# Performance work log

Measured on AMD Instinct MI355X. Metric: run time of the kernel, lower is better.

Reference implementation:

```python
import jax, jax.numpy as jnp
import numpy as np

B, H, W, C = 64, 56, 56, 256
ROUTES = 4
CONV_OUT = 64
BN_EPS = 1e-3  # keras BatchNormalization default epsilon


def setup_inputs() -> dict:
    key = jax.random.key(0)
    ks = jax.random.split(key, 8)
    inputs = jax.random.normal(ks[0], (B, H, W, C), jnp.float32)
    gamma = jnp.ones((C,), jnp.float32)
    beta = jnp.zeros((C,), jnp.float32)
    moving_mean = 0.1 * jax.random.normal(ks[1], (C,), jnp.float32)
    moving_var = jax.random.uniform(ks[2], (C,), jnp.float32, 0.5, 1.5)
    conv_w = 0.02 * jax.random.normal(ks[3], (3, 3, C, CONV_OUT), jnp.float32)  # HWIO
    conv_b = jnp.zeros((CONV_OUT,), jnp.float32)
    fc_w = 0.05 * jax.random.normal(ks[4], (CONV_OUT, ROUTES), jnp.float32)
    fc_b = jnp.zeros((ROUTES,), jnp.float32)
    return {"inputs": inputs, "gamma": gamma, "beta": beta,
            "moving_mean": moving_mean, "moving_var": moving_var,
            "conv_w": conv_w, "conv_b": conv_b, "fc_w": fc_w, "fc_b": fc_b}


def reference(inputs, gamma, beta, moving_mean, moving_var, conv_w, conv_b, fc_w, fc_b):
    # BatchNormalization in inference mode (training=None -> moving stats)
    rx = (inputs - moving_mean) * jax.lax.rsqrt(moving_var + BN_EPS) * gamma + beta
    # Conv2D(64, 3x3, stride 2, padding 'same'), NHWC / HWIO
    rx = jax.lax.conv_general_dilated(
        rx, conv_w, window_strides=(2, 2), padding="SAME",
        dimension_numbers=("NHWC", "HWIO", "NHWC")) + conv_b
    # GlobalAveragePooling2D -> [B, 64]
    rx = jnp.mean(rx, axis=(1, 2))
    # Dense(routes) -> routing logits [B, ROUTES]
    routing_x = rx @ fc_w + fc_b
    # choose_route: top-1 route, direct per-sample channel slice (no dense mask)
    route_width = C // ROUTES
    route = jnp.argmax(routing_x, axis=-1)  # [B]
    ch_idx = route[:, None] * route_width + jnp.arange(route_width)  # [B, rw]
    idx = ch_idx[:, None, None, :]  # [B,1,1,rw] broadcasts over H, W
    x = jnp.take_along_axis(inputs, idx, axis=3)  # [B, H, W, rw]
    return x, routing_x
```

## Files before the change

### kernel.cpp

```cpp
#include <hip/hip_runtime.h>

#define B 64
#define H 56
#define W 56
#define C 256
#define ROUTES 4
#define CONV_OUT 64
#define BN_EPS 0.001f
#define RW (C / ROUTES)
#define X_SIZE ((long)B * H * W * RW)

#define WS_FLOATS ((long)B * H * 3 * C)

typedef float floatx4 __attribute__((ext_vector_type(4)));

__device__ __forceinline__ void f4add(float4& a, const float4& v) {
    a.x += v.x; a.y += v.y; a.z += v.z; a.w += v.w;
}

__global__ __launch_bounds__(256) void k_reduce(const float* __restrict__ x,
                                                float* __restrict__ ws) {
    int blk = blockIdx.x;
    int tid = threadIdx.x;
    int cg = tid & 63;
    int wg = tid >> 6;

    const float4* xv = (const float4*)x;
    long base = (long)blk * W * (C / 4) + cg;

    float4 v[14];
    #pragma unroll
    for (int i = 0; i < 14; ++i) v[i] = xv[base + (long)(wg + 4 * i) * (C / 4)];

    float4 a = {0,0,0,0}, b4 = {0,0,0,0};
    #pragma unroll
    for (int i = 0; i < 14; i += 2) { f4add(a, v[i]); f4add(b4, v[i + 1]); }
    f4add(a, b4);

    __shared__ float4 lds[4][64];
    lds[wg][cg] = a;

    float4* w3 = (float4*)ws + (long)blk * 3 * (C / 4);
    if (wg == 0) w3[2 * (C / 4) + cg] = v[0];
    __syncthreads();
    if (wg == 0) {
        float4 e = lds[0][cg]; f4add(e, lds[2][cg]);
        w3[cg] = e;
    } else if (wg == 1) {
        float4 o = lds[1][cg]; f4add(o, lds[3][cg]);
        w3[C / 4 + cg] = o;
    }
}

__global__ __launch_bounds__(256) void k_route(const float* __restrict__ ws,
                                               const float* __restrict__ gamma,
                                               const float* __restrict__ beta,
                                               const float* __restrict__ mmean,
                                               const float* __restrict__ mvar,
                                               const float* __restrict__ conv_w,
                                               const float* __restrict__ conv_b,
                                               const float* __restrict__ fc_w,
                                               const float* __restrict__ fc_b,
                                               float* __restrict__ out_routing,
                                               int* __restrict__ route) {
    __shared__ float tl[9][C];
    __shared__ float part[4][CONV_OUT];
    __shared__ float cm[CONV_OUT];
    __shared__ float rxs[ROUTES];

    int b = blockIdx.x;
    int c = threadIdx.x;

    const float* base = ws + (long)b * H * 3 * C;
    float See = 0, Seo = 0, Soe = 0, Soo = 0, c0e = 0, c0o = 0;
    for (int h = 0; h < H; h += 2) {
        const float* pe = base + (long)h * 3 * C;
        const float* po = pe + 3 * C;
        See += pe[c];          Seo += pe[C + c];     c0e += pe[2 * C + c];
        Soe += po[c];          Soo += po[C + c];     c0o += po[2 * C + c];
    }
    float r0e = base[c];
    float r0o = base[C + c];
    float x00 = base[2 * C + c];

    float a  = gamma[c] * rsqrtf(mvar[c] + BN_EPS);
    float bb = beta[c] - mmean[c] * a;

    float Sx[9] = { See,             Seo,             See - c0e,
                    Soe,             Soo,             Soe - c0o,
                    See - r0e,       Seo - r0o,       See - r0e - c0e + x00 };
    const float cnt[9] = { 784.f, 784.f, 756.f,
                           784.f, 784.f, 756.f,
                           756.f, 756.f, 729.f };
    #pragma unroll
    for (int k = 0; k < 9; ++k) tl[k][c] = a * Sx[k] + bb * cnt[k];
    __syncthreads();

    int o = threadIdx.x & 63;
    int g = threadIdx.x >> 6;
    float p = 0.f;
    for (int cc = g * 64; cc < g * 64 + 64; ++cc) {
        #pragma unroll
        for (int k = 0; k < 9; ++k)
            p += tl[k][cc] * conv_w[(k * C + cc) * CONV_OUT + o];
    }
    part[g][o] = p;
    __syncthreads();

    if (threadIdx.x < CONV_OUT) {
        int o2 = threadIdx.x;
        float s = part[0][o2] + part[1][o2] + part[2][o2] + part[3][o2];
        cm[o2] = s * (1.f / 784.f) + conv_b[o2];
    }
    __syncthreads();

    if (threadIdx.x < ROUTES) {
        int r = threadIdx.x;
        float s = fc_b[r];
        for (int o2 = 0; o2 < CONV_OUT; ++o2) s += cm[o2] * fc_w[o2 * ROUTES + r];
        rxs[r] = s;
        out_routing[b * ROUTES + r] = s;
    }
    __syncthreads();

    if (threadIdx.x == 0) {
        int best = 0;
        for (int r = 1; r < ROUTES; ++r) if (rxs[r] > rxs[best]) best = r;
        route[b] = best;
    }
}

__global__ __launch_bounds__(256) void k_gather(const float* __restrict__ x,
                                                const int* __restrict__ route,
                                                float* __restrict__ out) {
    long idx = (long)blockIdx.x * blockDim.x + threadIdx.x;
    int j = (int)(idx & 15);
    long pixel = idx >> 4;
    int b = (int)(pixel / (H * W));
    const floatx4* xv = (const floatx4*)x;
    floatx4 v = xv[pixel * (C / 4) + (long)route[b] * (RW / 4) + j];
    __builtin_nontemporal_store(v, &((floatx4*)out)[idx]);
}

extern "C" void kernel_launch(void* const* d_in, const int* in_sizes, int n_in,
                              void* d_out, int out_size, void* d_ws, size_t ws_size,
                              hipStream_t stream) {
    const float* inputs = (const float*)d_in[0];
    const float* gamma  = (const float*)d_in[1];
    const float* beta   = (const float*)d_in[2];
    const float* mmean  = (const float*)d_in[3];
    const float* mvar   = (const float*)d_in[4];
    const float* conv_w = (const float*)d_in[5];
    const float* conv_b = (const float*)d_in[6];
    const float* fc_w   = (const float*)d_in[7];
    const float* fc_b   = (const float*)d_in[8];

    float* out   = (float*)d_out;
    float* ws    = (float*)d_ws;
    int*   route = (int*)((char*)d_ws + WS_FLOATS * sizeof(float));

    k_reduce<<<B * H, 256, 0, stream>>>(inputs, ws);
    k_route<<<B, 256, 0, stream>>>(ws, gamma, beta, mmean, mvar,
                                   conv_w, conv_b, fc_w, fc_b,
                                   out + X_SIZE, route);
    long n4 = X_SIZE / 4;
    k_gather<<<(int)(n4 / 256), 256, 0, stream>>>(inputs, route, out);
}
```

Before: 354.0 us.

## Fold conv and dense weights into per-channel route coefficients, atomically accumulate partial sums

Precomputes a fused weight that folds the conv weights through the dense layer and the BN scale, so each channel maps directly to four route logits. These weights are computed in four extra blocks of the reduce kernel. Per-row partial sums are accumulated with atomics into a compact per-batch 9xC buffer instead of a per-row workspace, which shrinks the route kernel to a short dot product and tree reduction. The gather kernel now does four vectors per thread and loads the route once per block. The atomic traffic and the added memset launch are the costs, and float atomics make the summation order nondeterministic.

New measurement: 331.2 us. 1.07x faster.

```diff
diff --git a/kernel.cpp b/kernel.cpp
--- a/kernel.cpp
+++ b/kernel.cpp
@@ -10,7 +10,10 @@
 #define RW (C / ROUTES)
 #define X_SIZE ((long)B * H * W * RW)
 
-#define WS_FLOATS ((long)B * H * 3 * C)
+#define P_FLOATS ((long)B * 9 * C)
+#define OFFU P_FLOATS
+#define U_FLOATS (10L * C * 4)
+#define OFFROUTE (OFFU + U_FLOATS)
 
 typedef float floatx4 __attribute__((ext_vector_type(4)));
 
@@ -19,9 +22,67 @@
 }
 
 __global__ __launch_bounds__(256) void k_reduce(const float* __restrict__ x,
+                                                const float* __restrict__ gamma,
+                                                const float* __restrict__ beta,
+                                                const float* __restrict__ mmean,
+                                                const float* __restrict__ mvar,
+                                                const float* __restrict__ conv_w,
+                                                const float* __restrict__ fc_w,
                                                 float* __restrict__ ws) {
+    int tid = threadIdx.x;
+
+    if (blockIdx.x >= B * H) {
+        __shared__ float fcw_s[CONV_OUT * ROUTES];
+        fcw_s[tid] = fc_w[tid];
+        __syncthreads();
+
+        int c = (blockIdx.x - B * H) * 64 + (tid >> 2);
+        int r = tid & 3;
+
+        float t[9];
+        #pragma unroll
+        for (int k = 0; k < 9; ++k) {
+            const float4* w4 = (const float4*)conv_w + ((long)(k * C + c) * CONV_OUT) / 4;
+            float s = 0.f;
+            #pragma unroll
+            for (int o4 = 0; o4 < 16; ++o4) {
+                float4 wv = w4[o4];
+                s += wv.x * fcw_s[(o4 * 4 + 0) * 4 + r];
+                s += wv.y * fcw_s[(o4 * 4 + 1) * 4 + r];
+                s += wv.z * fcw_s[(o4 * 4 + 2) * 4 + r];
+                s += wv.w * fcw_s[(o4 * 4 + 3) * 4 + r];
+            }
+            t[k] = s;
+        }
+
+        float a  = gamma[c] * rsqrtf(mvar[c] + BN_EPS);
+        float bb = beta[c] - mmean[c] * a;
+
+        float u[10];
+        u[0] =  t[0] + t[2] + t[6] + t[8];
+        u[1] =  t[1] + t[7];
+        u[2] =  t[3] + t[5];
+        u[3] =  t[4];
+        u[4] = -(t[2] + t[8]);
+        u[5] = -t[5];
+        u[6] = -(t[6] + t[8]);
+        u[7] = -t[7];
+        u[8] =  t[8];
+        u[9] = 784.f * (t[0] + t[1] + t[3] + t[4])
+             + 756.f * (t[2] + t[5] + t[6] + t[7])
+             + 729.f * t[8];
+
+        float* U = ws + OFFU;
+        float sa = a * (1.f / 784.f);
+        #pragma unroll
+        for (int j = 0; j < 9; ++j) U[(j * C + c) * 4 + r] = sa * u[j];
+        U[(9 * C + c) * 4 + r] = bb * (1.f / 784.f) * u[9];
+        return;
+    }
+
     int blk = blockIdx.x;
-    int tid = threadIdx.x;
+    int b = blk / H;
+    int h = blk % H;
     int cg = tid & 63;
     int wg = tid >> 6;
 
@@ -32,98 +93,70 @@
     #pragma unroll
     for (int i = 0; i < 14; ++i) v[i] = xv[base + (long)(wg + 4 * i) * (C / 4)];
 
-    float4 a = {0,0,0,0}, b4 = {0,0,0,0};
-    #pragma unroll
-    for (int i = 0; i < 14; i += 2) { f4add(a, v[i]); f4add(b4, v[i + 1]); }
-    f4add(a, b4);
+    float4 a4 = {0,0,0,0}, b4 = {0,0,0,0};
+    #pragma unroll
+    for (int i = 0; i < 14; i += 2) { f4add(a4, v[i]); f4add(b4, v[i + 1]); }
+    f4add(a4, b4);
 
     __shared__ float4 lds[4][64];
-    lds[wg][cg] = a;
-
-    float4* w3 = (float4*)ws + (long)blk * 3 * (C / 4);
-    if (wg == 0) w3[2 * (C / 4) + cg] = v[0];
+    lds[wg][cg] = a4;
     __syncthreads();
+
+    float* Pb = ws + (long)b * 9 * C;
+    int c0 = cg * 4;
+    int hp = h & 1;
+    #define ATOM4(j, q) { float* p = Pb + (j) * C + c0; \
+        atomicAdd(p+0, (q).x); atomicAdd(p+1, (q).y); \
+        atomicAdd(p+2, (q).z); atomicAdd(p+3, (q).w); }
+
     if (wg == 0) {
         float4 e = lds[0][cg]; f4add(e, lds[2][cg]);
-        w3[cg] = e;
+        ATOM4(hp * 2, e);
+        ATOM4(4 + hp, v[0]);
+        if (h == 0) { ATOM4(6, e); ATOM4(8, v[0]); }
     } else if (wg == 1) {
         float4 o = lds[1][cg]; f4add(o, lds[3][cg]);
-        w3[C / 4 + cg] = o;
-    }
+        ATOM4(hp * 2 + 1, o);
+        if (h == 0) ATOM4(7, o);
+    }
+    #undef ATOM4
 }
 
 __global__ __launch_bounds__(256) void k_route(const float* __restrict__ ws,
-                                               const float* __restrict__ gamma,
-                                               const float* __restrict__ beta,
-                                               const float* __restrict__ mmean,
-                                               const float* __restrict__ mvar,
-                                               const float* __restrict__ conv_w,
                                                const float* __restrict__ conv_b,
                                                const float* __restrict__ fc_w,
                                                const float* __restrict__ fc_b,
                                                float* __restrict__ out_routing,
                                                int* __restrict__ route) {
-    __shared__ float tl[9][C];
-    __shared__ float part[4][CONV_OUT];
-    __shared__ float cm[CONV_OUT];
+    __shared__ floatx4 red[256];
     __shared__ float rxs[ROUTES];
 
     int b = blockIdx.x;
     int c = threadIdx.x;
-
-    const float* base = ws + (long)b * H * 3 * C;
-    float See = 0, Seo = 0, Soe = 0, Soo = 0, c0e = 0, c0o = 0;
-    for (int h = 0; h < H; h += 2) {
-        const float* pe = base + (long)h * 3 * C;
-        const float* po = pe + 3 * C;
-        See += pe[c];          Seo += pe[C + c];     c0e += pe[2 * C + c];
-        Soe += po[c];          Soo += po[C + c];     c0o += po[2 * C + c];
-    }
-    float r0e = base[c];
-    float r0o = base[C + c];
-    float x00 = base[2 * C + c];
-
-    float a  = gamma[c] * rsqrtf(mvar[c] + BN_EPS);
-    float bb = beta[c] - mmean[c] * a;
-
-    float Sx[9] = { See,             Seo,             See - c0e,
-                    Soe,             Soo,             Soe - c0o,
-                    See - r0e,       Seo - r0o,       See - r0e - c0e + x00 };
-    const float cnt[9] = { 784.f, 784.f, 756.f,
-                           784.f, 784.f, 756.f,
-                           756.f, 756.f, 729.f };
-    #pragma unroll
-    for (int k = 0; k < 9; ++k) tl[k][c] = a * Sx[k] + bb * cnt[k];
+    const float* Pb = ws + (long)b * 9 * C;
+    const floatx4* U4 = (const floatx4*)(ws + OFFU);
+
+    floatx4 v = U4[9 * C + c];
+    #pragma unroll
+    for (int j = 0; j < 9; ++j) v += Pb[j * C + c] * U4[j * C + c];
+
+    red[c] = v;
     __syncthreads();
-
-    int o = threadIdx.x & 63;
-    int g = threadIdx.x >> 6;
-    float p = 0.f;
-    for (int cc = g * 64; cc < g * 64 + 64; ++cc) {
-        #pragma unroll
-        for (int k = 0; k < 9; ++k)
-            p += tl[k][cc] * conv_w[(k * C + cc) * CONV_OUT + o];
-    }
-    part[g][o] = p;
+    #pragma unroll
+    for (int s = 128; s >= 1; s >>= 1) {
+        if (c < s) red[c] += red[c + s];
+        __syncthreads();
+    }
+
+    if (c < ROUTES) {
+        float cst = fc_b[c];
+        for (int o = 0; o < CONV_OUT; ++o) cst += conv_b[o] * fc_w[o * ROUTES + c];
+        float val = red[0][c] + cst;
+        rxs[c] = val;
+        out_routing[b * ROUTES + c] = val;
+    }
     __syncthreads();
-
-    if (threadIdx.x < CONV_OUT) {
-        int o2 = threadIdx.x;
-        float s = part[0][o2] + part[1][o2] + part[2][o2] + part[3][o2];
-        cm[o2] = s * (1.f / 784.f) + conv_b[o2];
-    }
-    __syncthreads();
-
-    if (threadIdx.x < ROUTES) {
-        int r = threadIdx.x;
-        float s = fc_b[r];
-        for (int o2 = 0; o2 < CONV_OUT; ++o2) s += cm[o2] * fc_w[o2 * ROUTES + r];
-        rxs[r] = s;
-        out_routing[b * ROUTES + r] = s;
-    }
-    __syncthreads();
-
-    if (threadIdx.x == 0) {
+    if (c == 0) {
         int best = 0;
         for (int r = 1; r < ROUTES; ++r) if (rxs[r] > rxs[best]) best = r;
         route[b] = best;
@@ -133,13 +166,18 @@
 __global__ __launch_bounds__(256) void k_gather(const float* __restrict__ x,
                                                 const int* __restrict__ route,
                                                 float* __restrict__ out) {
-    long idx = (long)blockIdx.x * blockDim.x + threadIdx.x;
-    int j = (int)(idx & 15);
-    long pixel = idx >> 4;
-    int b = (int)(pixel / (H * W));
+    long base4 = (long)blockIdx.x * 1024 + threadIdx.x;
+    int b = blockIdx.x / 49;
+    int rt = route[b];
     const floatx4* xv = (const floatx4*)x;
-    floatx4 v = xv[pixel * (C / 4) + (long)route[b] * (RW / 4) + j];
-    __builtin_nontemporal_store(v, &((floatx4*)out)[idx]);
+    #pragma unroll
+    for (int m = 0; m < 4; ++m) {
+        long idx = base4 + m * 256;
+        int j = (int)(idx & 15);
+        long pixel = idx >> 4;
+        floatx4 v = xv[pixel * (C / 4) + (long)rt * (RW / 4) + j];
+        __builtin_nontemporal_store(v, &((floatx4*)out)[idx]);
+    }
 }
 
 extern "C" void kernel_launch(void* const* d_in, const int* in_sizes, int n_in,
@@ -157,12 +195,12 @@
 
     float* out   = (float*)d_out;
     float* ws    = (float*)d_ws;
-    int*   route = (int*)((char*)d_ws + WS_FLOATS * sizeof(float));
-
-    k_reduce<<<B * H, 256, 0, stream>>>(inputs, ws);
-    k_route<<<B, 256, 0, stream>>>(ws, gamma, beta, mmean, mvar,
-                                   conv_w, conv_b, fc_w, fc_b,
-                                   out + X_SIZE, route);
-    long n4 = X_SIZE / 4;
-    k_gather<<<(int)(n4 / 256), 256, 0, stream>>>(inputs, route, out);
-}
+    int*   route = (int*)((char*)d_ws + OFFROUTE * sizeof(float));
+
+    hipMemsetAsync(d_ws, 0, P_FLOATS * sizeof(float), stream);
+
+    k_reduce<<<B * H + 4, 256, 0, stream>>>(inputs, gamma, beta, mmean, mvar,
+                                            conv_w, fc_w, ws);
+    k_route<<<B, 256, 0, stream>>>(ws, conv_b, fc_w, fc_b, out + X_SIZE, route);
+    k_gather<<<3136, 256, 0, stream>>>(inputs, route, out);
+}
```
